# Optimization experiments

Measured on AMD Instinct MI355X. Metric: run time of the kernel, lower is better.

Reference implementation:

```python
import jax, jax.numpy as jnp
import numpy as np

B, N, D = 64, 100, 32            # batch, nodes, node feature size
FE = [96, 160, 192]              # edge-MLP layer sizes
FN = [256, 256, 32]              # node-MLP layer sizes
ALPHA = 0.2                      # leaky relu slope


def _lin_init(key, fan_in, fan_out):
    kw, kb = jax.random.split(key)
    bound = 1.0 / np.sqrt(fan_in)
    w = jax.random.uniform(kw, (fan_in, fan_out), jnp.float32, -bound, bound)
    b = jax.random.uniform(kb, (fan_out,), jnp.float32, -bound, bound)
    return w, b


def setup_inputs() -> dict:
    key = jax.random.key(0)
    ks = jax.random.split(key, 7)
    d = {"x": jax.random.normal(ks[0], (B, N, D), jnp.float32)}
    fe_sizes = [2 * D] + FE                    # edge MLP: in = concat(x_i, x_j)
    fn_sizes = [FE[-1] + D] + FN               # node MLP: in = concat(agg, x)
    for li in range(3):
        w, b = _lin_init(ks[1 + li], fe_sizes[li], fe_sizes[li + 1])
        d[f"fe_w{li}"], d[f"fe_b{li}"] = w, b
    for li in range(3):
        w, b = _lin_init(ks[4 + li], fn_sizes[li], fn_sizes[li + 1])
        d[f"fn_w{li}"], d[f"fn_b{li}"] = w, b
    return d


def reference(x, fe_w0, fe_b0, fe_w1, fe_b1, fe_w2, fe_b2,
              fn_w0, fn_b0, fn_w1, fn_b1, fn_w2, fn_b2):
    b, n, d = x.shape
    lr = lambda v: jax.nn.leaky_relu(v, ALPHA)
    # fully-connected pairwise edge features: A[b,i,j] = concat(x_i, x_j)
    xi = jnp.broadcast_to(x[:, :, None, :], (b, n, n, d))
    xj = jnp.broadcast_to(x[:, None, :, :], (b, n, n, d))
    a = jnp.concatenate([xi, xj], axis=-1)          # [b, n, n, 2d]
    # edge MLP (fe): leaky relu after every layer (final_linear=False)
    a = lr(a @ fe_w0 + fe_b0)
    a = lr(a @ fe_w1 + fe_b1)
    a = lr(a @ fe_w2 + fe_b2)                       # [b, n, n, FE[-1]]
    # sum aggregation over neighbors j
    agg = jnp.sum(a, axis=2)                        # [b, n, FE[-1]]
    # node MLP (fn): final layer linear (final_linear=True)
    h = jnp.concatenate([agg, x], axis=-1)          # [b, n, FE[-1]+d]
    h = lr(h @ fn_w0 + fn_b0)
    h = lr(h @ fn_w1 + fn_b1)
    h = h @ fn_w2 + fn_b2                           # [b, n, FN[-1]]
    return h
```

## Files before the change

### kernel.cpp

```cpp
#include <hip/hip_runtime.h>

#define B_    64
#define N_    100
#define D_    32
#define F0    96
#define F1    160
#define F2    192
#define HID   256
#define FOUT  32

typedef unsigned short u16;
typedef unsigned int   u32;
typedef u16   u16x8 __attribute__((ext_vector_type(8)));
typedef __bf16 bf16x8 __attribute__((ext_vector_type(8)));
typedef __bf16 bf16x2 __attribute__((ext_vector_type(2)));
typedef float  fx4   __attribute__((ext_vector_type(4)));

__device__ __forceinline__ u16 f2bfu(float f) {
    u32 u = __float_as_uint(f);
    u += 0x7fffu + ((u >> 16) & 1u);
    return (u16)(u >> 16);
}
#if __has_builtin(__builtin_amdgcn_cvt_pk_bf16_f32)
__device__ __forceinline__ u32 pk2(float a, float b) {
    bf16x2 t = __builtin_amdgcn_cvt_pk_bf16_f32(a, b);
    return __builtin_bit_cast(u32, t);
}
#else
__device__ __forceinline__ u32 pk2(float a, float b) {
    return (u32)f2bfu(a) | ((u32)f2bfu(b) << 16);
}
#endif
__device__ __forceinline__ float lrelu(float v) { return fmaxf(v, 0.2f * v); }

__device__ __forceinline__ bf16x8 fragLds(const u16* p) {
    return __builtin_bit_cast(bf16x8, *(const u16x8*)p);
}
__device__ __forceinline__ bf16x8 fragGbl(const u16* __restrict__ p) {
    return __builtin_bit_cast(bf16x8, *(const u16x8*)p);
}
#define MFMA(a, b, c) __builtin_amdgcn_mfma_f32_16x16x32_bf16((a), (b), (c), 0, 0, 0)

#define OFF_P     0u
#define OFF_V     2457600u
#define OFF_AGG   4915200u
#define OFF_PACK  7372800u
#define PK_W1     0
#define PK_W2     15360
#define PK_N0     46080
#define PK_N1     103424
#define PK_N2     168960
#define PK_TOTAL  177152

#define PV_BLOCKS 2400
#define PACK_BLOCKS 346

__global__ __launch_bounds__(512) void prep_kernel(
    const float* __restrict__ x,
    const float* __restrict__ few0, const float* __restrict__ feb0,
    const float* __restrict__ few1, const float* __restrict__ few2,
    const float* __restrict__ fnw0, const float* __restrict__ fnw1,
    const float* __restrict__ fnw2,
    float* __restrict__ P, float* __restrict__ V, u16* __restrict__ wpack)
{
    const int blk = blockIdx.x, tid = threadIdx.x;
    if (blk < PV_BLOCKS) {
        int o = blk * 512 + tid;
        int r = o / 192, h = o - r * 192;
        const float* xr = x + r * D_;
        if (h < F0) {
            float acc = feb0[h];
            #pragma unroll
            for (int d = 0; d < D_; ++d) acc = fmaf(xr[d], few0[d * F0 + h], acc);
            P[r * F0 + h] = acc;
        } else {
            int k = h - F0;
            float acc = 0.f;
            #pragma unroll
            for (int d = 0; d < D_; ++d) acc = fmaf(xr[d], few0[(D_ + d) * F0 + k], acc);
            V[r * F0 + k] = acc;
        }
    } else {
        int p = (blk - PV_BLOCKS) * 512 + tid;
        const float* src; int start, Ncols, NT;
        if (p < PK_W2)      { start = PK_W1; src = few1; Ncols = F1;   NT = 10; }
        else if (p < PK_N0) { start = PK_W2; src = few2; Ncols = F2;   NT = 12; }
        else if (p < PK_N1) { start = PK_N0; src = fnw0; Ncols = HID;  NT = 16; }
        else if (p < PK_N2) { start = PK_N1; src = fnw1; Ncols = HID;  NT = 16; }
        else                { start = PK_N2; src = fnw2; Ncols = FOUT; NT = 2;  }
        int local = p - start;
        int j = local & 7, lane = (local >> 3) & 63, rest = local >> 9;
        int nt = rest % NT, kt = rest / NT;
        int n = 16 * nt + (lane & 15);
        int k = 32 * kt + 8 * (lane >> 4) + j;
        wpack[p] = f2bfu(src[k * Ncols + n]);
    }
}

__global__ __launch_bounds__(512, 4) void edge_kernel(
    const float* __restrict__ P, const float* __restrict__ V,
    const u16* __restrict__ W1p, const u16* __restrict__ W2p,
    const float* __restrict__ feb1, const float* __restrict__ feb2,
    u16* __restrict__ agg)
{
    const int i = blockIdx.x, b = blockIdx.y;
    const int tid = threadIdx.x, ld = tid & 63, wv = tid >> 6;
    const int c = ld & 15, Q = ld >> 4;
    const int row = b * N_ + i;

    __shared__ __align__(16) u16  sB0[3 * 7 * 64 * 8];
    __shared__ __align__(16) u16  sB1[5 * 7 * 64 * 8];
    __shared__ __align__(16) float sP[F0];
    __shared__ __align__(16) float sAggP[2 * F2];

    if (tid < 24) ((float4*)sP)[tid] = ((const float4*)(P + (size_t)row * F0))[tid];
    __syncthreads();

    {
        const float* Vb = V + (size_t)b * (N_ * F0);
        #pragma unroll
        for (int s = 0; s < 3; ++s) {
            int o = tid + 512 * s;
            if (o < 1344) {
                int mt = o / 192;
                int rem = o - mt * 192;
                int kt = rem >> 6, lane = rem & 63;
                int m = 16 * mt + (lane & 15);
                int kb = 32 * kt + 8 * (lane >> 4);
                const float* vp = Vb + m * F0 + kb;
                float4 va = *(const float4*)vp;
                float4 vb = *(const float4*)(vp + 4);
                float4 pa = *(const float4*)&sP[kb];
                float4 pb = *(const float4*)&sP[kb + 4];
                uint4 w;
                w.x = pk2(lrelu(pa.x + va.x), lrelu(pa.y + va.y));
                w.y = pk2(lrelu(pa.z + va.z), lrelu(pa.w + va.w));
                w.z = pk2(lrelu(pb.x + vb.x), lrelu(pb.y + vb.y));
                w.w = pk2(lrelu(pb.z + vb.z), lrelu(pb.w + vb.w));
                *(uint4*)&sB0[o * 8] = w;
            }
        }
    }
    __syncthreads();

    {
        const int wf = wv >> 2, wm = wv & 3, ftb = wf * 5;
        #pragma unroll
        for (int mi = 0; mi < 2; ++mi) {
            const int mt = wm + 4 * mi;
            if (mt < 7) {
                bf16x8 b0[3];
                #pragma unroll
                for (int kt = 0; kt < 3; ++kt)
                    b0[kt] = fragLds(sB0 + ((mt * 3 + kt) * 64 + ld) * 8);
                #pragma unroll
                for (int t = 0; t < 5; ++t) {
                    const int ft = ftb + t;
                    fx4 acc = (fx4){0.f, 0.f, 0.f, 0.f};
                    #pragma unroll
                    for (int kt = 0; kt < 3; ++kt) {
                        bf16x8 aw = fragGbl(W1p + (size_t)((kt * 10 + ft) * 64 + ld) * 8);
                        acc = MFMA(aw, b0[kt], acc);
                    }
                    const int f0 = 16 * ft + 4 * Q;
                    float4 bias = *(const float4*)(feb1 + f0);
                    u32 lo = pk2(lrelu(acc[0] + bias.x), lrelu(acc[1] + bias.y));
                    u32 hi = pk2(lrelu(acc[2] + bias.z), lrelu(acc[3] + bias.w));
                    const int kt2 = f0 >> 5, o8 = (f0 >> 3) & 3, j0 = f0 & 7;
                    *(uint2*)&sB1[((mt * 5 + kt2) * 64 + c + 16 * o8) * 8 + j0] = (uint2){lo, hi};
                }
            }
        }
    }
    __syncthreads();

    {
        const int wf2 = wv >> 1, wm2 = wv & 1;
        float ag[3][4];
        #pragma unroll
        for (int t = 0; t < 3; ++t)
            #pragma unroll
            for (int r = 0; r < 4; ++r) ag[t][r] = 0.f;

        #pragma unroll
        for (int mi = 0; mi < 4; ++mi) {
            const int mt = wm2 + 2 * mi;
            if (mt < 7) {
                bf16x8 b1[5];
                #pragma unroll
                for (int kt = 0; kt < 5; ++kt)
                    b1[kt] = fragLds(sB1 + ((mt * 5 + kt) * 64 + ld) * 8);
                #pragma unroll
                for (int t = 0; t < 3; ++t) {
                    const int ft = wf2 + 4 * t;
                    fx4 acc = (fx4){0.f, 0.f, 0.f, 0.f};
                    #pragma unroll
                    for (int kt = 0; kt < 5; ++kt) {
                        bf16x8 aw = fragGbl(W2p + (size_t)((kt * 12 + ft) * 64 + ld) * 8);
                        acc = MFMA(aw, b1[kt], acc);
                    }
                    const int f0 = 16 * ft + 4 * Q;
                    float4 bias = *(const float4*)(feb2 + f0);
                    const bool pad = (mt == 6) && (c >= 4);
                    ag[t][0] += pad ? 0.f : lrelu(acc[0] + bias.x);
                    ag[t][1] += pad ? 0.f : lrelu(acc[1] + bias.y);
                    ag[t][2] += pad ? 0.f : lrelu(acc[2] + bias.z);
                    ag[t][3] += pad ? 0.f : lrelu(acc[3] + bias.w);
                }
            }
        }
        #pragma unroll
        for (int t = 0; t < 3; ++t)
            #pragma unroll
            for (int r = 0; r < 4; ++r) {
                float v = ag[t][r];
                v += __shfl_xor(v, 1);
                v += __shfl_xor(v, 2);
                v += __shfl_xor(v, 4);
                v += __shfl_xor(v, 8);
                ag[t][r] = v;
            }
        if (c == 0) {
            #pragma unroll
            for (int t = 0; t < 3; ++t) {
                float4 vv = {ag[t][0], ag[t][1], ag[t][2], ag[t][3]};
                *(float4*)&sAggP[wm2 * F2 + 16 * (wf2 + 4 * t) + 4 * Q] = vv;
            }
        }
    }
    __syncthreads();

    if (tid < F2)
        agg[(size_t)row * F2 + tid] = f2bfu(sAggP[tid] + sAggP[F2 + tid]);
}

__global__ __launch_bounds__(512, 4) void node_kernel(
    const u16* __restrict__ agg, const float* __restrict__ x,
    const u16* __restrict__ n0p, const u16* __restrict__ n1p,
    const u16* __restrict__ n2p,
    const float* __restrict__ fnb0, const float* __restrict__ fnb1,
    const float* __restrict__ fnb2,
    float* __restrict__ out)
{
    const int blk = blockIdx.x;
    const int tid = threadIdx.x, ld = tid & 63, wv = tid >> 6;
    const int c = ld & 15, Q = ld >> 4;

    __shared__ __align__(16) u16 sH0p[7 * 512];
    __shared__ __align__(16) u16 sH1p[8 * 512];
    __shared__ __align__(16) u16 sH2p[8 * 512];

    if (tid < 448) {
        int kt = tid >> 6, lane = tid & 63;
        int m = lane & 15;
        int kb = 32 * kt + 8 * (lane >> 4);
        int g = 16 * blk + m;
        uint4 w;
        if (kb < F2) {
            w = *(const uint4*)(agg + (size_t)g * F2 + kb);
        } else {
            const float* xp = x + (size_t)g * D_ + (kb - F2);
            float4 a = *(const float4*)xp;
            float4 bb = *(const float4*)(xp + 4);
            w.x = pk2(a.x, a.y);  w.y = pk2(a.z, a.w);
            w.z = pk2(bb.x, bb.y); w.w = pk2(bb.z, bb.w);
        }
        *(uint4*)&sH0p[tid * 8] = w;
    }
    __syncthreads();

    {
        fx4 acc[2];
        #pragma unroll
        for (int t = 0; t < 2; ++t) acc[t] = (fx4){0.f, 0.f, 0.f, 0.f};
        for (int kt = 0; kt < 7; ++kt) {
            bf16x8 a = fragLds(sH0p + (kt * 64 + ld) * 8);
            #pragma unroll
            for (int t = 0; t < 2; ++t) {
                bf16x8 bw = fragGbl(n0p + (size_t)((kt * 16 + wv + 8 * t) * 64 + ld) * 8);
                acc[t] = MFMA(a, bw, acc[t]);
            }
        }
        #pragma unroll
        for (int t = 0; t < 2; ++t) {
            int f = 16 * (wv + 8 * t) + c;
            float bias = fnb0[f];
            int kt2 = f >> 5, o8 = (f >> 3) & 3, j2 = f & 7;
            #pragma unroll
            for (int r = 0; r < 4; ++r) {
                float val = lrelu(acc[t][r] + bias);
                sH1p[((kt2) * 64 + (4 * Q + r) + 16 * o8) * 8 + j2] = f2bfu(val);
            }
        }
    }
    __syncthreads();

    {
        fx4 acc[2];
        #pragma unroll
        for (int t = 0; t < 2; ++t) acc[t] = (fx4){0.f, 0.f, 0.f, 0.f};
        for (int kt = 0; kt < 8; ++kt) {
            bf16x8 a = fragLds(sH1p + (kt * 64 + ld) * 8);
            #pragma unroll
            for (int t = 0; t < 2; ++t) {
                bf16x8 bw = fragGbl(n1p + (size_t)((kt * 16 + wv + 8 * t) * 64 + ld) * 8);
                acc[t] = MFMA(a, bw, acc[t]);
            }
        }
        #pragma unroll
        for (int t = 0; t < 2; ++t) {
            int f = 16 * (wv + 8 * t) + c;
            float bias = fnb1[f];
            int kt2 = f >> 5, o8 = (f >> 3) & 3, j2 = f & 7;
            #pragma unroll
            for (int r = 0; r < 4; ++r) {
                float val = lrelu(acc[t][r] + bias);
                sH2p[((kt2) * 64 + (4 * Q + r) + 16 * o8) * 8 + j2] = f2bfu(val);
            }
        }
    }
    __syncthreads();

    if (wv < 2) {
        int nt = wv;
        fx4 acc = (fx4){0.f, 0.f, 0.f, 0.f};
        for (int kt = 0; kt < 8; ++kt) {
            bf16x8 a = fragLds(sH2p + (kt * 64 + ld) * 8);
            bf16x8 bw = fragGbl(n2p + (size_t)((kt * 2 + nt) * 64 + ld) * 8);
            acc = MFMA(a, bw, acc);
        }
        int f = 16 * nt + c;
        float bias = fnb2[f];
        #pragma unroll
        for (int r = 0; r < 4; ++r) {
            int g = 16 * blk + 4 * Q + r;
            out[(size_t)g * FOUT + f] = acc[r] + bias;
        }
    }
}

extern "C" void kernel_launch(void* const* d_in, const int* in_sizes, int n_in,
                              void* d_out, int out_size, void* d_ws, size_t ws_size,
                              hipStream_t stream) {
    const float* x    = (const float*)d_in[0];
    const float* few0 = (const float*)d_in[1];
    const float* feb0 = (const float*)d_in[2];
    const float* few1 = (const float*)d_in[3];
    const float* feb1 = (const float*)d_in[4];
    const float* few2 = (const float*)d_in[5];
    const float* feb2 = (const float*)d_in[6];
    const float* fnw0 = (const float*)d_in[7];
    const float* fnb0 = (const float*)d_in[8];
    const float* fnw1 = (const float*)d_in[9];
    const float* fnb1 = (const float*)d_in[10];
    const float* fnw2 = (const float*)d_in[11];
    const float* fnb2 = (const float*)d_in[12];

    char* w = (char*)d_ws;
    float* P    = (float*)(w + OFF_P);
    float* V    = (float*)(w + OFF_V);
    u16*   agg  = (u16*)(w + OFF_AGG);
    u16*   pack = (u16*)(w + OFF_PACK);

    prep_kernel<<<PV_BLOCKS + PACK_BLOCKS, 512, 0, stream>>>(
        x, few0, feb0, few1, few2, fnw0, fnw1, fnw2, P, V, pack);

    edge_kernel<<<dim3(N_, B_), 512, 0, stream>>>(
        P, V, pack + PK_W1, pack + PK_W2, feb1, feb2, agg);

    node_kernel<<<400, 512, 0, stream>>>(
        agg, x, pack + PK_N0, pack + PK_N1, pack + PK_N2,
        fnb0, fnb1, fnb2, (float*)d_out);
}
```

Baseline: 228.9 us.

## Build layer-0 edge fragments in registers and swap MFMA operand roles

The edge kernel no longer stages the first-layer activations in shared memory. Each wave builds its bf16 A-fragments directly from V and P in registers, which removes one LDS buffer and one barrier. MFMA operands are swapped so edge rows act as A and weights as B, biases are preloaded into the accumulators, and the neighbour sum becomes a cross-lane shuffle over Q. Occupancy is raised to 8 waves per SIMD through launch bounds, which risks register pressure. The node kernel now processes 8 rows per block over 800 blocks, wasting half of each MFMA tile but doubling the number of blocks.

```diff
diff --git a/kernel.cpp b/kernel.cpp
--- a/kernel.cpp
+++ b/kernel.cpp
@@ -54,6 +54,8 @@
 
 #define PV_BLOCKS 2400
 #define PACK_BLOCKS 346
+#define NODE_ROWS 8
+#define NODE_BLOCKS 800
 
 __global__ __launch_bounds__(512) void prep_kernel(
     const float* __restrict__ x,
@@ -97,7 +99,7 @@
     }
 }
 
-__global__ __launch_bounds__(512, 4) void edge_kernel(
+__global__ __launch_bounds__(512, 8) void edge_kernel(
     const float* __restrict__ P, const float* __restrict__ V,
     const u16* __restrict__ W1p, const u16* __restrict__ W2p,
     const float* __restrict__ feb1, const float* __restrict__ feb2,
@@ -108,66 +110,59 @@
     const int c = ld & 15, Q = ld >> 4;
     const int row = b * N_ + i;
 
-    __shared__ __align__(16) u16  sB0[3 * 7 * 64 * 8];
-    __shared__ __align__(16) u16  sB1[5 * 7 * 64 * 8];
+    __shared__ __align__(16) u16  sA1p[7 * 5 * 64 * 8];
     __shared__ __align__(16) float sP[F0];
     __shared__ __align__(16) float sAggP[2 * F2];
 
     if (tid < 24) ((float4*)sP)[tid] = ((const float4*)(P + (size_t)row * F0))[tid];
     __syncthreads();
 
+    const int wn = wv & 3, wm = wv >> 2;
+
     {
+        const int nCnt = (wn < 2) ? 3 : 2;
         const float* Vb = V + (size_t)b * (N_ * F0);
-        #pragma unroll
-        for (int s = 0; s < 3; ++s) {
-            int o = tid + 512 * s;
-            if (o < 1344) {
-                int mt = o / 192;
-                int rem = o - mt * 192;
-                int kt = rem >> 6, lane = rem & 63;
-                int m = 16 * mt + (lane & 15);
-                int kb = 32 * kt + 8 * (lane >> 4);
-                const float* vp = Vb + m * F0 + kb;
-                float4 va = *(const float4*)vp;
-                float4 vb = *(const float4*)(vp + 4);
-                float4 pa = *(const float4*)&sP[kb];
-                float4 pb = *(const float4*)&sP[kb + 4];
-                uint4 w;
-                w.x = pk2(lrelu(pa.x + va.x), lrelu(pa.y + va.y));
-                w.y = pk2(lrelu(pa.z + va.z), lrelu(pa.w + va.w));
-                w.z = pk2(lrelu(pb.x + vb.x), lrelu(pb.y + vb.y));
-                w.w = pk2(lrelu(pb.z + vb.z), lrelu(pb.w + vb.w));
-                *(uint4*)&sB0[o * 8] = w;
-            }
-        }
-    }
-    __syncthreads();
-
-    {
-        const int wf = wv >> 2, wm = wv & 3, ftb = wf * 5;
-        #pragma unroll
-        for (int mi = 0; mi < 2; ++mi) {
-            const int mt = wm + 4 * mi;
+        float bias[3];
+        #pragma unroll
+        for (int t = 0; t < 3; ++t) if (t < nCnt) bias[t] = feb1[16 * (wn + 4 * t) + c];
+
+        #pragma unroll
+        for (int mi = 0; mi < 4; ++mi) {
+            const int mt = 4 * wm + mi;
             if (mt < 7) {
-                bf16x8 b0[3];
+                const int m = 16 * mt + c;
+                const int mc = (m < N_) ? m : (N_ - 1);
+                const float* vp = Vb + mc * F0;
+                bf16x8 a[3];
                 #pragma unroll
-                for (int kt = 0; kt < 3; ++kt)
-                    b0[kt] = fragLds(sB0 + ((mt * 3 + kt) * 64 + ld) * 8);
+                for (int kt = 0; kt < 3; ++kt) {
+                    const int kb = 32 * kt + 8 * Q;
+                    float4 va = *(const float4*)(vp + kb);
+                    float4 vb2 = *(const float4*)(vp + kb + 4);
+                    float4 pa = *(const float4*)&sP[kb];
+                    float4 pb = *(const float4*)&sP[kb + 4];
+                    uint4 w;
+                    w.x = pk2(lrelu(pa.x + va.x), lrelu(pa.y + va.y));
+                    w.y = pk2(lrelu(pa.z + va.z), lrelu(pa.w + va.w));
+                    w.z = pk2(lrelu(pb.x + vb2.x), lrelu(pb.y + vb2.y));
+                    w.w = pk2(lrelu(pb.z + vb2.z), lrelu(pb.w + vb2.w));
+                    a[kt] = __builtin_bit_cast(bf16x8, w);
+                }
                 #pragma unroll
-                for (int t = 0; t < 5; ++t) {
-                    const int ft = ftb + t;
-                    fx4 acc = (fx4){0.f, 0.f, 0.f, 0.f};
+                for (int t = 0; t < 3; ++t) if (t < nCnt) {
+                    const int nt = wn + 4 * t;
+                    fx4 acc = (fx4){bias[t], bias[t], bias[t], bias[t]};
                     #pragma unroll
                     for (int kt = 0; kt < 3; ++kt) {
-                        bf16x8 aw = fragGbl(W1p + (size_t)((kt * 10 + ft) * 64 + ld) * 8);
-                        acc = MFMA(aw, b0[kt], acc);
+                        bf16x8 bw = fragGbl(W1p + (size_t)((kt * 10 + nt) * 64 + ld) * 8);
+                        acc = MFMA(a[kt], bw, acc);
                     }
-                    const int f0 = 16 * ft + 4 * Q;
-                    float4 bias = *(const float4*)(feb1 + f0);
-                    u32 lo = pk2(lrelu(acc[0] + bias.x), lrelu(acc[1] + bias.y));
-                    u32 hi = pk2(lrelu(acc[2] + bias.z), lrelu(acc[3] + bias.w));
-                    const int kt2 = f0 >> 5, o8 = (f0 >> 3) & 3, j0 = f0 & 7;
-                    *(uint2*)&sB1[((mt * 5 + kt2) * 64 + c + 16 * o8) * 8 + j0] = (uint2){lo, hi};
+                    const int f = 16 * nt + c;
+                    const int kt2 = f >> 5, lq = (f >> 3) & 3, j2 = f & 7;
+                    #pragma unroll
+                    for (int r = 0; r < 4; ++r)
+                        sA1p[((mt * 5 + kt2) * 64 + (4 * Q + r) + 16 * lq) * 8 + j2] =
+                            f2bfu(lrelu(acc[r]));
                 }
             }
         }
@@ -175,57 +170,43 @@
     __syncthreads();
 
     {
-        const int wf2 = wv >> 1, wm2 = wv & 1;
-        float ag[3][4];
-        #pragma unroll
-        for (int t = 0; t < 3; ++t)
-            #pragma unroll
-            for (int r = 0; r < 4; ++r) ag[t][r] = 0.f;
+        float aggp[3] = {0.f, 0.f, 0.f};
+        float bias2[3];
+        #pragma unroll
+        for (int t = 0; t < 3; ++t) bias2[t] = feb2[16 * (wn + 4 * t) + c];
 
         #pragma unroll
         for (int mi = 0; mi < 4; ++mi) {
-            const int mt = wm2 + 2 * mi;
+            const int mt = 4 * wm + mi;
             if (mt < 7) {
-                bf16x8 b1[5];
+                bf16x8 a[5];
                 #pragma unroll
                 for (int kt = 0; kt < 5; ++kt)
-                    b1[kt] = fragLds(sB1 + ((mt * 5 + kt) * 64 + ld) * 8);
+                    a[kt] = fragLds(sA1p + ((mt * 5 + kt) * 64 + ld) * 8);
+                const bool ok = (mt < 6) || (Q == 0);
                 #pragma unroll
                 for (int t = 0; t < 3; ++t) {
-                    const int ft = wf2 + 4 * t;
-                    fx4 acc = (fx4){0.f, 0.f, 0.f, 0.f};
+                    const int nt = wn + 4 * t;
+                    fx4 acc = (fx4){bias2[t], bias2[t], bias2[t], bias2[t]};
                     #pragma unroll
                     for (int kt = 0; kt < 5; ++kt) {
-                        bf16x8 aw = fragGbl(W2p + (size_t)((kt * 12 + ft) * 64 + ld) * 8);
-                        acc = MFMA(aw, b1[kt], acc);
+                        bf16x8 bw = fragGbl(W2p + (size_t)((kt * 12 + nt) * 64 + ld) * 8);
+                        acc = MFMA(a[kt], bw, acc);
                     }
-                    const int f0 = 16 * ft + 4 * Q;
-                    float4 bias = *(const float4*)(feb2 + f0);
-                    const bool pad = (mt == 6) && (c >= 4);
-                    ag[t][0] += pad ? 0.f : lrelu(acc[0] + bias.x);
-                    ag[t][1] += pad ? 0.f : lrelu(acc[1] + bias.y);
-                    ag[t][2] += pad ? 0.f : lrelu(acc[2] + bias.z);
-                    ag[t][3] += pad ? 0.f : lrelu(acc[3] + bias.w);
+                    if (ok)
+                        aggp[t] += lrelu(acc[0]) + lrelu(acc[1]) + lrelu(acc[2]) + lrelu(acc[3]);
                 }
             }
         }
         #pragma unroll
-        for (int t = 0; t < 3; ++t)
-            #pragma unroll
-            for (int r = 0; r < 4; ++r) {
-                float v = ag[t][r];
-                v += __shfl_xor(v, 1);
-                v += __shfl_xor(v, 2);
-                v += __shfl_xor(v, 4);
-                v += __shfl_xor(v, 8);
-                ag[t][r] = v;
-            }
-        if (c == 0) {
-            #pragma unroll
-            for (int t = 0; t < 3; ++t) {
-                float4 vv = {ag[t][0], ag[t][1], ag[t][2], ag[t][3]};
-                *(float4*)&sAggP[wm2 * F2 + 16 * (wf2 + 4 * t) + 4 * Q] = vv;
-            }
+        for (int t = 0; t < 3; ++t) {
+            aggp[t] += __shfl_xor(aggp[t], 16, 64);
+            aggp[t] += __shfl_xor(aggp[t], 32, 64);
+        }
+        if (ld < 16) {
+            #pragma unroll
+            for (int t = 0; t < 3; ++t)
+                sAggP[wm * F2 + 16 * (wn + 4 * t) + ld] = aggp[t];
         }
     }
     __syncthreads();
@@ -254,7 +235,7 @@
         int kt = tid >> 6, lane = tid & 63;
         int m = lane & 15;
         int kb = 32 * kt + 8 * (lane >> 4);
-        int g = 16 * blk + m;
+        int g = NODE_ROWS * blk + ((m < NODE_ROWS) ? m : (NODE_ROWS - 1));
         uint4 w;
         if (kb < F2) {
             w = *(const uint4*)(agg + (size_t)g * F2 + kb);
@@ -329,12 +310,14 @@
             bf16x8 bw = fragGbl(n2p + (size_t)((kt * 2 + nt) * 64 + ld) * 8);
             acc = MFMA(a, bw, acc);
         }
-        int f = 16 * nt + c;
-        float bias = fnb2[f];
-        #pragma unroll
-        for (int r = 0; r < 4; ++r) {
-            int g = 16 * blk + 4 * Q + r;
-            out[(size_t)g * FOUT + f] = acc[r] + bias;
+        if (Q < 2) {
+            int f = 16 * nt + c;
+            float bias = fnb2[f];
+            #pragma unroll
+            for (int r = 0; r < 4; ++r) {
+                int g = NODE_ROWS * blk + 4 * Q + r;
+                out[(size_t)g * FOUT + f] = acc[r] + bias;
+            }
         }
     }
 }
@@ -368,7 +351,7 @@
     edge_kernel<<<dim3(N_, B_), 512, 0, stream>>>(
         P, V, pack + PK_W1, pack + PK_W2, feb1, feb2, agg);
 
-    node_kernel<<<400, 512, 0, stream>>>(
+    node_kernel<<<NODE_BLOCKS, 512, 0, stream>>>(
         agg, x, pack + PK_N0, pack + PK_N1, pack + PK_N2,
         fnb0, fnb1, fnb2, (float*)d_out);
 }
```

Measured after the change: 331.0 us. 1.45x slower.
